# Performance work log

Measured on AMD Instinct MI355X. Metric: run time of the kernel, lower is better.

## Reference

```python
import jax, jax.numpy as jnp
import numpy as np

EMBED_DIM = 1024
VALUE_DIM = 2048
NUM_HEADS = 8
KEY_DIM = EMBED_DIM // NUM_HEADS      # 128
HEAD_DIM = VALUE_DIM // NUM_HEADS     # 256
B, T = 2, 2048
EPS = 1e-6


def _rotate_every_two(x):
    # x: [..., d] with d even; pairs (x0,x1)->(-x1,x0)
    x1 = x[..., ::2]
    x2 = x[..., 1::2]
    return jnp.stack((-x2, x1), axis=-1).reshape(x.shape)


def _theta_shift(x, sin, cos):
    # sin/cos: [T, key_dim] broadcast over [B, H, T, key_dim]
    return x * cos + _rotate_every_two(x) * sin


def setup_inputs() -> dict:
    key = jax.random.key(0)
    ks = jax.random.split(key, 6)
    x = jax.random.normal(ks[0], (B, T, EMBED_DIM), dtype=jnp.float32)

    # rotary angles as in torchscale RetNetRelPos
    angle = 1.0 / (10000.0 ** jnp.linspace(0.0, 1.0, KEY_DIM // 2))
    angle = jnp.repeat(angle, 2)                       # [key_dim], interleaved pairs
    idx = jnp.arange(T, dtype=jnp.float32)
    sin = jnp.sin(idx[:, None] * angle[None, :])       # [T, key_dim]
    cos = jnp.cos(idx[:, None] * angle[None, :])

    # per-head decay mask, normalized by sqrt(row-sum) as in RetNet
    decay = jnp.log(1.0 - 2.0 ** (-5.0 - jnp.arange(NUM_HEADS, dtype=jnp.float32)))
    diff = idx[:, None] - idx[None, :]                 # [T, T]
    exponent = jnp.where(diff >= 0, decay[:, None, None] * diff[None], -jnp.inf)
    mask = jnp.exp(exponent)                           # [H, T, T], lower-triangular decay
    mask = mask / jnp.sqrt(mask.sum(-1, keepdims=True))

    s = 0.02
    Wq = s * jax.random.normal(ks[1], (EMBED_DIM, EMBED_DIM), dtype=jnp.float32)
    Wk = s * jax.random.normal(ks[2], (EMBED_DIM, EMBED_DIM), dtype=jnp.float32)
    Wv = s * jax.random.normal(ks[3], (EMBED_DIM, VALUE_DIM), dtype=jnp.float32)
    Wg = s * jax.random.normal(ks[4], (EMBED_DIM, VALUE_DIM), dtype=jnp.float32)
    Wo = s * jax.random.normal(ks[5], (VALUE_DIM, EMBED_DIM), dtype=jnp.float32)
    return {"x": x, "sin": sin, "cos": cos, "mask": mask,
            "Wq": Wq, "Wk": Wk, "Wv": Wv, "Wg": Wg, "Wo": Wo}


def reference(x, sin, cos, mask, Wq, Wk, Wv, Wg, Wo):
    bsz, tgt_len, _ = x.shape
    scaling = KEY_DIM ** (-0.5)

    q = x @ Wq
    k = (x @ Wk) * scaling
    v = x @ Wv
    g = x @ Wg

    q = q.reshape(bsz, tgt_len, NUM_HEADS, KEY_DIM).transpose(0, 2, 1, 3)  # [B,H,T,kd]
    k = k.reshape(bsz, tgt_len, NUM_HEADS, KEY_DIM).transpose(0, 2, 1, 3)
    qr = _theta_shift(q, sin, cos)
    kr = _theta_shift(k, sin, cos)

    vr = v.reshape(bsz, tgt_len, NUM_HEADS, HEAD_DIM).transpose(0, 2, 1, 3)  # [B,H,T,hd]

    # parallel retention: decay-masked QK^T with abs-sum normalization (detached)
    qk = jnp.einsum('bhtd,bhsd->bhts', qr, kr) * mask[None]
    denom = jnp.clip(jnp.sum(jnp.abs(jax.lax.stop_gradient(qk)), axis=-1, keepdims=True),
                     1.0, 50000.0)
    qk = qk / denom
    out = jnp.einsum('bhts,bhsd->bhtd', qk, vr)          # [B,H,T,hd]
    out = out.transpose(0, 2, 1, 3)                      # [B,T,H,hd]

    # per-head RMSNorm (no affine)
    out = out * jax.lax.rsqrt(jnp.mean(out * out, axis=-1, keepdims=True) + EPS)
    out = out.reshape(bsz, tgt_len, VALUE_DIM)

    out = jax.nn.silu(g) * out
    return out @ Wo
```

## Files before the change

### kernel.cpp

```cpp
#include <hip/hip_runtime.h>
#include <hip/hip_bf16.h>
#include <math.h>

constexpr int T_SEQ = 2048;
constexpr int BB    = 2;
constexpr int EMBED = 1024;
constexpr int VDIM  = 2048;
constexpr int NHEADS = 8;
constexpr int KDIM  = 128;
constexpr int HDIM  = 256;
constexpr int ROWS  = BB * T_SEQ;
constexpr int NALL  = 6144;
constexpr float EPS = 1e-6f;

typedef float  f32x4  __attribute__((ext_vector_type(4)));
typedef __bf16 bf16x8 __attribute__((ext_vector_type(8)));
typedef __bf16 bf16x4 __attribute__((ext_vector_type(4)));

__device__ __forceinline__ void gload16(const void* g, void* l) {
    __builtin_amdgcn_global_load_lds(
        (__attribute__((address_space(1))) void*)g,
        (__attribute__((address_space(3))) void*)l, 16, 0, 0);
}

__global__ __launch_bounds__(256)
void prep_all(const float* __restrict__ x, const float* __restrict__ Wq,
              const float* __restrict__ Wk, const float* __restrict__ Wv,
              const float* __restrict__ Wg, const float* __restrict__ Wo,
              __bf16* __restrict__ xb,
              __bf16* __restrict__ WqT, __bf16* __restrict__ WkT,
              __bf16* __restrict__ WvT, __bf16* __restrict__ WgT,
              __bf16* __restrict__ WoT) {
    const int bid = blockIdx.x;
    const int x_ = threadIdx.x, y_ = threadIdx.y;
    if (bid >= 8192) {
        const int i = (bid - 8192) * 256 + y_ * 32 + x_;
        float4 v = reinterpret_cast<const float4*>(x)[i];
        bf16x4 o = { (__bf16)v.x, (__bf16)v.y, (__bf16)v.z, (__bf16)v.w };
        reinterpret_cast<bf16x4*>(xb)[i] = o;
        return;
    }
    const float* W; __bf16* WT; int K, N, cx, cy;
    if (bid < 1024)      { W = Wq; WT = WqT; K = 1024; N = 1024; int rm = bid;        cx = rm & 31; cy = rm >> 5; }
    else if (bid < 2048) { W = Wk; WT = WkT; K = 1024; N = 1024; int rm = bid - 1024; cx = rm & 31; cy = rm >> 5; }
    else if (bid < 4096) { W = Wv; WT = WvT; K = 1024; N = 2048; int rm = bid - 2048; cx = rm & 63; cy = rm >> 6; }
    else if (bid < 6144) { W = Wg; WT = WgT; K = 1024; N = 2048; int rm = bid - 4096; cx = rm & 63; cy = rm >> 6; }
    else                 { W = Wo; WT = WoT; K = 2048; N = 1024; int rm = bid - 6144; cx = rm & 31; cy = rm >> 5; }

    __shared__ float tile[32][33];
    const int c0 = cx * 32, k0 = cy * 32;
    #pragma unroll
    for (int p = 0; p < 4; ++p)
        tile[y_ + p * 8][x_] = W[(size_t)(k0 + y_ + p * 8) * N + c0 + x_];
    __syncthreads();
    #pragma unroll
    for (int p = 0; p < 4; ++p)
        WT[(size_t)(c0 + y_ + p * 8) * K + k0 + x_] = (__bf16)tile[x_][y_ + p * 8];
}

__global__ __launch_bounds__(256)
void gemm_qkvg(const __bf16* __restrict__ A, const __bf16* __restrict__ BT,
               __bf16* __restrict__ Qb, __bf16* __restrict__ Kb,
               __bf16* __restrict__ Vt, __bf16* __restrict__ Gb,
               const float* __restrict__ sinT, const float* __restrict__ cosT) {
    constexpr int K = EMBED;
    __shared__ __align__(16) char smem[36864];
    __bf16* As = (__bf16*)smem;
    __bf16* Bs = (__bf16*)(smem + 16384);

    const int bid = blockIdx.x;
    const int swzb = (bid & 7) * 192 + (bid >> 3);
    const int rowBase = (swzb / 48) * 128;
    const int colBase = (swzb % 48) * 128;

    const int tid = threadIdx.x;
    const int w = tid >> 6, lane = tid & 63;
    const int g = lane >> 4, r = lane & 15;
    const int wm = w >> 1, wn = w & 1;

    const int vr  = lane >> 3;
    const int swz = ((lane & 7) ^ vr) * 8;
    const __bf16* aSb = A  + (size_t)(rowBase + 32 * w + vr) * K + swz;
    const __bf16* bSb = BT + (size_t)(colBase + 32 * w + vr) * K + swz;

    f32x4 acc[4][4];
    #pragma unroll
    for (int i = 0; i < 4; ++i)
        #pragma unroll
        for (int j = 0; j < 4; ++j)
            acc[i][j] = (f32x4){0.f, 0.f, 0.f, 0.f};

    for (int k0 = 0; k0 < K; k0 += 64) {
        __syncthreads();
        #pragma unroll
        for (int p = 0; p < 4; ++p) {
            const int cc = 4 * w + p;
            gload16(aSb + (size_t)(8 * p) * K + k0, smem         + cc * 1024);
            gload16(bSb + (size_t)(8 * p) * K + k0, smem + 16384 + cc * 1024);
        }
        __syncthreads();

        #pragma unroll
        for (int kk = 0; kk < 2; ++kk) {
            bf16x8 bfrag[4];
            #pragma unroll
            for (int nf = 0; nf < 4; ++nf) {
                const int row = wn * 64 + nf * 16 + r;
                bfrag[nf] = *reinterpret_cast<const bf16x8*>(
                    &Bs[row * 64 + (((kk << 2) + g) ^ (r & 7)) * 8]);
            }
            #pragma unroll
            for (int mf = 0; mf < 4; ++mf) {
                const int row = wm * 64 + mf * 16 + r;
                bf16x8 a = *reinterpret_cast<const bf16x8*>(
                    &As[row * 64 + (((kk << 2) + g) ^ (r & 7)) * 8]);
                #pragma unroll
                for (int nf = 0; nf < 4; ++nf)
                    acc[mf][nf] = __builtin_amdgcn_mfma_f32_16x16x32_bf16(a, bfrag[nf], acc[mf][nf], 0, 0, 0);
            }
        }
    }

    constexpr float kscale = 0.08838834764831845f;
    if (colBase >= 2048 && colBase < 4096) {
        __syncthreads();
        __bf16* Es = (__bf16*)smem + w * (64 * 72);
        #pragma unroll
        for (int mf = 0; mf < 4; ++mf)
            #pragma unroll
            for (int nf = 0; nf < 4; ++nf) {
                bf16x4 v = { (__bf16)acc[mf][nf][0], (__bf16)acc[mf][nf][1],
                             (__bf16)acc[mf][nf][2], (__bf16)acc[mf][nf][3] };
                *reinterpret_cast<bf16x4*>(&Es[(nf * 16 + r) * 72 + mf * 16 + g * 4]) = v;
            }
        __syncthreads();
        const int t0g = rowBase + wm * 64;
        const int bq = t0g >> 11, tl = t0g & 2047;
        const int colV0 = (colBase - 2048) + wn * 64;
        const int h = colV0 >> 8, dd0 = colV0 & 255;
        const int li = lane & 7, rgrp = lane >> 3;
        __bf16* vtb = Vt + ((size_t)(bq * NHEADS + h) * HDIM + dd0) * T_SEQ + tl;
        #pragma unroll
        for (int c = 0; c < 8; ++c) {
            const int drow = 8 * c + rgrp;
            bf16x8 v = *reinterpret_cast<const bf16x8*>(&Es[drow * 72 + li * 8]);
            *reinterpret_cast<bf16x8*>(vtb + (size_t)drow * T_SEQ + li * 8) = v;
        }
        return;
    }

    __bf16* dst; int dstride, cofs; float alphaSeg; bool rot;
    if (colBase < 1024)      { dst = Qb; dstride = 1024; cofs = colBase;        alphaSeg = 1.0f;   rot = true;  }
    else if (colBase < 2048) { dst = Kb; dstride = 1024; cofs = colBase - 1024; alphaSeg = kscale; rot = true;  }
    else                     { dst = Gb; dstride = 2048; cofs = colBase - 4096; alphaSeg = 1.0f;   rot = false; }

    #pragma unroll
    for (int mf = 0; mf < 4; ++mf)
        #pragma unroll
        for (int nf = 0; nf < 4; ++nf)
            #pragma unroll
            for (int j = 0; j < 4; ++j) {
                const int row  = rowBase + wm * 64 + mf * 16 + g * 4 + j;
                const int colL = cofs + wn * 64 + nf * 16 + r;
                float v = acc[mf][nf][j] * alphaSeg;
                if (rot) {
                    const float p = __shfl_xor(v, 1);
                    const int t  = row & (T_SEQ - 1);
                    const int dh = colL & (KDIM - 1);
                    const float c = cosT[t * KDIM + dh];
                    const float s = sinT[t * KDIM + dh];
                    v = (r & 1) ? (v * c + p * s) : (v * c - p * s);
                }
                dst[(size_t)row * dstride + colL] = (__bf16)v;
            }
}

__global__ __launch_bounds__(256)
void gemm_wo(const __bf16* __restrict__ A, const __bf16* __restrict__ BT,
             float* __restrict__ C) {
    constexpr int N = EMBED, K = VDIM;
    __shared__ __align__(16) char smem[24576];
    __bf16* As = (__bf16*)smem;
    __bf16* Bs = (__bf16*)(smem + 8192);

    const int bid = blockIdx.x;
    const int swzb = (bid & 7) * 64 + (bid >> 3);
    const int rowBase = (swzb >> 3) * 64;
    const int colBase = (swzb & 7) * 128;

    const int tid = threadIdx.x;
    const int w = tid >> 6, lane = tid & 63;
    const int g = lane >> 4, r = lane & 15;
    const int wm = w >> 1, wn = w & 1;

    const int vr  = lane >> 3;
    const int swz = ((lane & 7) ^ vr) * 8;
    const __bf16* aSb = A  + (size_t)(rowBase + 16 * w + vr) * K + swz;
    const __bf16* bSb = BT + (size_t)(colBase + 32 * w + vr) * K + swz;

    f32x4 acc[2][4];
    #pragma unroll
    for (int i = 0; i < 2; ++i)
        #pragma unroll
        for (int j = 0; j < 4; ++j)
            acc[i][j] = (f32x4){0.f, 0.f, 0.f, 0.f};

    for (int k0 = 0; k0 < K; k0 += 64) {
        __syncthreads();
        #pragma unroll
        for (int p = 0; p < 2; ++p) {
            const int cc = 2 * w + p;
            gload16(aSb + (size_t)(8 * p) * K + k0, smem + cc * 1024);
        }
        #pragma unroll
        for (int p = 0; p < 4; ++p) {
            const int cc = 4 * w + p;
            gload16(bSb + (size_t)(8 * p) * K + k0, smem + 8192 + cc * 1024);
        }
        __syncthreads();

        #pragma unroll
        for (int kk = 0; kk < 2; ++kk) {
            bf16x8 bfrag[4];
            #pragma unroll
            for (int nf = 0; nf < 4; ++nf) {
                const int row = wn * 64 + nf * 16 + r;
                bfrag[nf] = *reinterpret_cast<const bf16x8*>(
                    &Bs[row * 64 + (((kk << 2) + g) ^ (r & 7)) * 8]);
            }
            #pragma unroll
            for (int mf = 0; mf < 2; ++mf) {
                const int row = wm * 32 + mf * 16 + r;
                bf16x8 a = *reinterpret_cast<const bf16x8*>(
                    &As[row * 64 + (((kk << 2) + g) ^ (r & 7)) * 8]);
                #pragma unroll
                for (int nf = 0; nf < 4; ++nf)
                    acc[mf][nf] = __builtin_amdgcn_mfma_f32_16x16x32_bf16(a, bfrag[nf], acc[mf][nf], 0, 0, 0);
            }
        }
    }

    #pragma unroll
    for (int mf = 0; mf < 2; ++mf)
        #pragma unroll
        for (int nf = 0; nf < 4; ++nf)
            #pragma unroll
            for (int j = 0; j < 4; ++j) {
                const int row = rowBase + wm * 32 + mf * 16 + g * 4 + j;
                const int col = colBase + wn * 64 + nf * 16 + r;
                C[(size_t)row * N + col] = acc[mf][nf][j];
            }
}

__global__ __launch_bounds__(256)
void retention_mfma(const __bf16* __restrict__ Qb, const __bf16* __restrict__ Kb,
                    const __bf16* __restrict__ Vt,
                    const __bf16* __restrict__ Gb, __bf16* __restrict__ Yb) {
    const int tid = threadIdx.x;
    const int w = tid >> 6, lane = tid & 63;
    const int g = lane >> 4, r = lane & 15;
    const int rx = r & 7;
    const int bid = blockIdx.x;
    const int h = bid & 7;
    const int slot = bid >> 3;
    const int b = slot & 1;
    const int x = slot >> 1;
    const int qt = (b == 0) ? (31 - x) : x;
    const int tt0 = qt * 64;
    const int trow0 = w * 16;

    __shared__ __align__(16) __bf16 Ks[64][128];
    __shared__ __align__(16) __bf16 Vs[256][64];
    __shared__ __align__(16) __bf16 Ps[4][16][72];

    const float rho   = 1.0f - exp2f(-(float)(5 + h));
    const float l2r   = log2f(rho);
    const float inv1m = exp2f((float)(5 + h));
    int   tj[4];
    float nrm[4];
    #pragma unroll
    for (int j = 0; j < 4; ++j) {
        tj[j] = tt0 + trow0 + g * 4 + j;
        nrm[j] = rsqrtf((1.0f - exp2f(l2r * (float)(tj[j] + 1))) * inv1m);
    }
    float pneg[4];
    #pragma unroll
    for (int ssub = 0; ssub < 4; ++ssub)
        pneg[ssub] = exp2f(-l2r * (float)(ssub * 16 + r));

    bf16x8 qf[4];
    {
        const __bf16* qrow = Qb + ((size_t)(b * T_SEQ + tt0 + trow0 + r)) * EMBED + h * KDIM;
        #pragma unroll
        for (int kb = 0; kb < 4; ++kb)
            qf[kb] = *reinterpret_cast<const bf16x8*>(qrow + kb * 32 + g * 8);
    }

    f32x4 acc[16];
    #pragma unroll
    for (int db = 0; db < 16; ++db) acc[db] = (f32x4){0.f, 0.f, 0.f, 0.f};
    float dsum[4] = {0.f, 0.f, 0.f, 0.f};

    const __bf16* vtbase = Vt + ((size_t)(b * NHEADS + h) * HDIM) * T_SEQ;
    const __bf16* kbase  = Kb + ((size_t)(b * T_SEQ)) * EMBED + h * KDIM;

    const int klr = lane >> 4;
    const int kc  = lane & 15;
    const int kswz_even = (kc ^ klr) * 8;
    const int kswz_odd  = (kc ^ (4 + klr)) * 8;
    const int vlr  = lane >> 3;
    const int vswz = ((lane & 7) ^ vlr) * 8;

    const int nS = qt + 1;
    for (int st = 0; st < nS; ++st) {
        const int ss0 = st * 64;
        __syncthreads();
        #pragma unroll
        for (int p = 0; p < 4; ++p) {
            const int cc = 4 * w + p;
            const int se = (p & 1) ? kswz_odd : kswz_even;
            gload16(kbase + (size_t)(ss0 + 4 * cc + klr) * EMBED + se,
                    (char*)&Ks[0][0] + cc * 1024);
        }
        #pragma unroll
        for (int p = 0; p < 8; ++p) {
            const int cc = 8 * w + p;
            gload16(vtbase + (size_t)(8 * cc + vlr) * T_SEQ + ss0 + vswz,
                    (char*)&Vs[0][0] + cc * 1024);
        }
        __syncthreads();

        float wj[4];
        #pragma unroll
        for (int j = 0; j < 4; ++j)
            wj[j] = exp2f(l2r * (float)(tj[j] - ss0)) * nrm[j];
        const bool diag = (st == qt);

        #pragma unroll
        for (int ssub = 0; ssub < 4; ++ssub) {
            f32x4 sacc = (f32x4){0.f, 0.f, 0.f, 0.f};
            #pragma unroll
            for (int kb = 0; kb < 4; ++kb) {
                bf16x8 kf = *reinterpret_cast<const bf16x8*>(
                    &Ks[ssub * 16 + r][((kb * 4 + g) ^ rx) * 8]);
                sacc = __builtin_amdgcn_mfma_f32_16x16x32_bf16(qf[kb], kf, sacc, 0, 0, 0);
            }
            const int scol = ss0 + ssub * 16 + r;
            const float mfac = pneg[ssub];
            #pragma unroll
            for (int j = 0; j < 4; ++j) {
                float pv = sacc[j] * (wj[j] * mfac);
                if (diag && scol > tj[j]) pv = 0.f;
                dsum[j] += fabsf(pv);
                Ps[w][g * 4 + j][ssub * 16 + r] = (__bf16)pv;
            }
        }

        #pragma unroll
        for (int sh = 0; sh < 2; ++sh) {
            bf16x8 pf = *reinterpret_cast<const bf16x8*>(&Ps[w][r][sh * 32 + g * 8]);
            #pragma unroll
            for (int db = 0; db < 16; ++db) {
                bf16x8 vf = *reinterpret_cast<const bf16x8*>(
                    &Vs[db * 16 + r][((sh * 4 + g) ^ rx) * 8]);
                acc[db] = __builtin_amdgcn_mfma_f32_16x16x32_bf16(pf, vf, acc[db], 0, 0, 0);
            }
        }
    }

    #pragma unroll
    for (int j = 0; j < 4; ++j) {
        float v = dsum[j];
        v += __shfl_xor(v, 1); v += __shfl_xor(v, 2);
        v += __shfl_xor(v, 4); v += __shfl_xor(v, 8);
        dsum[j] = fminf(fmaxf(v, 1.0f), 50000.0f);
    }
    float ss[4] = {0.f, 0.f, 0.f, 0.f};
    #pragma unroll
    for (int db = 0; db < 16; ++db)
        #pragma unroll
        for (int j = 0; j < 4; ++j) {
            const float v = acc[db][j] / dsum[j];
            acc[db][j] = v;
            ss[j] = fmaf(v, v, ss[j]);
        }
    #pragma unroll
    for (int j = 0; j < 4; ++j) {
        float v = ss[j];
        v += __shfl_xor(v, 1); v += __shfl_xor(v, 2);
        v += __shfl_xor(v, 4); v += __shfl_xor(v, 8);
        ss[j] = rsqrtf(v * (1.0f / 256.0f) + EPS);
    }
    #pragma unroll
    for (int j = 0; j < 4; ++j) {
        const size_t row = (size_t)(b * T_SEQ + tj[j]);
        const __bf16* grow = Gb + row * VDIM + h * HDIM;
        __bf16* yrow = Yb + row * VDIM + h * HDIM;
        #pragma unroll
        for (int db = 0; db < 16; ++db) {
            const int c = db * 16 + r;
            const float gv = (float)grow[c];
            const float sil = gv / (1.0f + expf(-gv));
            yrow[c] = (__bf16)(sil * acc[db][j] * ss[j]);
        }
    }
}

extern "C" void kernel_launch(void* const* d_in, const int* in_sizes, int n_in,
                              void* d_out, int out_size, void* d_ws, size_t ws_size,
                              hipStream_t stream) {
    (void)in_sizes; (void)n_in; (void)out_size; (void)ws_size;

    const float* x    = (const float*)d_in[0];
    const float* sinT = (const float*)d_in[1];
    const float* cosT = (const float*)d_in[2];
    const float* Wq   = (const float*)d_in[4];
    const float* Wk   = (const float*)d_in[5];
    const float* Wv   = (const float*)d_in[6];
    const float* Wg   = (const float*)d_in[7];
    const float* Wo   = (const float*)d_in[8];
    float* out = (float*)d_out;

    char* wsp = (char*)d_ws;
    __bf16* xb  = (__bf16*)(wsp);
    __bf16* WqT = (__bf16*)(wsp + (8u  << 20));
    __bf16* WkT = (__bf16*)(wsp + (10u << 20));
    __bf16* WvT = (__bf16*)(wsp + (12u << 20));
    __bf16* WgT = (__bf16*)(wsp + (16u << 20));
    __bf16* WoT = (__bf16*)(wsp + (20u << 20));
    __bf16* Qb  = (__bf16*)(wsp + (24u << 20));
    __bf16* Kb  = (__bf16*)(wsp + (32u << 20));
    __bf16* Yb  = (__bf16*)(wsp + (40u << 20));
    __bf16* Gb  = (__bf16*)(wsp + (56u << 20));
    __bf16* Vt  = (__bf16*)(wsp + (72u << 20));
    __bf16* WTall = WqT;

    const dim3 blk(256);
    const dim3 tblk(32, 8);

    prep_all<<<12288, tblk, 0, stream>>>(x, Wq, Wk, Wv, Wg, Wo,
                                         xb, WqT, WkT, WvT, WgT, WoT);

    gemm_qkvg<<<1536, blk, 0, stream>>>(xb, WTall, Qb, Kb, Vt, Gb, sinT, cosT);

    retention_mfma<<<512, blk, 0, stream>>>(Qb, Kb, Vt, Gb, Yb);

    gemm_wo<<<512, blk, 0, stream>>>(Yb, WoT, out);
}
```

Before: 194.7 us.

## Double-buffer K tiles and overlap V load with QK^T in retention kernel

Moves the K tile to a double-buffered shared array, prefetching the next K tile while the current one is consumed. The V tile load is issued before the QK^T MFMAs and only waited on afterwards, using explicit vmcnt waits and raw barriers. This hides global-to-LDS latency behind compute, at the cost of extra LDS and hand-managed wait counts that must match the number of outstanding loads.

```diff
diff --git a/kernel.cpp b/kernel.cpp
--- a/kernel.cpp
+++ b/kernel.cpp
@@ -22,6 +22,9 @@
         (__attribute__((address_space(1))) void*)g,
         (__attribute__((address_space(3))) void*)l, 16, 0, 0);
 }
+
+#define WAITV(n) asm volatile("s_waitcnt vmcnt(" #n ")" ::: "memory")
+#define BARRIER() __builtin_amdgcn_s_barrier()
 
 __global__ __launch_bounds__(256)
 void prep_all(const float* __restrict__ x, const float* __restrict__ Wq,
@@ -269,7 +272,7 @@
     const int tt0 = qt * 64;
     const int trow0 = w * 16;
 
-    __shared__ __align__(16) __bf16 Ks[64][128];
+    __shared__ __align__(16) __bf16 Ks[2][64][128];
     __shared__ __align__(16) __bf16 Vs[256][64];
     __shared__ __align__(16) __bf16 Ps[4][16][72];
 
@@ -311,24 +314,38 @@
     const int vlr  = lane >> 3;
     const int vswz = ((lane & 7) ^ vlr) * 8;
 
+    #pragma unroll
+    for (int p = 0; p < 4; ++p) {
+        const int cc = 4 * w + p;
+        const int se = (p & 1) ? kswz_odd : kswz_even;
+        gload16(kbase + (size_t)(4 * cc + klr) * EMBED + se,
+                (char*)&Ks[0][0][0] + cc * 1024);
+    }
+
+    int cur = 0;
     const int nS = qt + 1;
     for (int st = 0; st < nS; ++st) {
         const int ss0 = st * 64;
-        __syncthreads();
-        #pragma unroll
-        for (int p = 0; p < 4; ++p) {
-            const int cc = 4 * w + p;
-            const int se = (p & 1) ? kswz_odd : kswz_even;
-            gload16(kbase + (size_t)(ss0 + 4 * cc + klr) * EMBED + se,
-                    (char*)&Ks[0][0] + cc * 1024);
-        }
+        WAITV(0);
+        BARRIER();
+
         #pragma unroll
         for (int p = 0; p < 8; ++p) {
             const int cc = 8 * w + p;
             gload16(vtbase + (size_t)(8 * cc + vlr) * T_SEQ + ss0 + vswz,
                     (char*)&Vs[0][0] + cc * 1024);
         }
-        __syncthreads();
+        const bool more = (st + 1 < nS);
+        if (more) {
+            const int ssn = ss0 + 64;
+            #pragma unroll
+            for (int p = 0; p < 4; ++p) {
+                const int cc = 4 * w + p;
+                const int se = (p & 1) ? kswz_odd : kswz_even;
+                gload16(kbase + (size_t)(ssn + 4 * cc + klr) * EMBED + se,
+                        (char*)&Ks[cur ^ 1][0][0] + cc * 1024);
+            }
+        }
 
         float wj[4];
         #pragma unroll
@@ -342,7 +359,7 @@
             #pragma unroll
             for (int kb = 0; kb < 4; ++kb) {
                 bf16x8 kf = *reinterpret_cast<const bf16x8*>(
-                    &Ks[ssub * 16 + r][((kb * 4 + g) ^ rx) * 8]);
+                    &Ks[cur][ssub * 16 + r][((kb * 4 + g) ^ rx) * 8]);
                 sacc = __builtin_amdgcn_mfma_f32_16x16x32_bf16(qf[kb], kf, sacc, 0, 0, 0);
             }
             const int scol = ss0 + ssub * 16 + r;
@@ -356,6 +373,10 @@
             }
         }
 
+        if (more) { WAITV(4); }
+        else      { WAITV(0); }
+        BARRIER();
+
         #pragma unroll
         for (int sh = 0; sh < 2; ++sh) {
             bf16x8 pf = *reinterpret_cast<const bf16x8*>(&Ps[w][r][sh * 32 + g * 8]);
@@ -366,6 +387,7 @@
                 acc[db] = __builtin_amdgcn_mfma_f32_16x16x32_bf16(pf, vf, acc[db], 0, 0, 0);
             }
         }
+        cur ^= 1;
     }
 
     #pragma unroll
```

Measured after the change: 191.5 us. No clear change (-1.6%).
